# Optimization experiments

Measured on AMD Instinct MI355X. Metric: run time of the kernel, lower is better.

The kernel has to match this reference:

```python
import jax, jax.numpy as jnp
import numpy as np

HEADS = 8

def setup_inputs() -> dict:
    key = jax.random.key(0)
    ks = jax.random.split(key, 5)
    B, C, H, W = 2, 256, 64, 64
    dim = C
    x = jax.random.normal(ks[0], (B, C, H, W), dtype=jnp.float32)
    # Linear weights stored as [in, out] so y = x @ W + b
    w_qkv = jax.random.normal(ks[1], (dim, 3 * dim), dtype=jnp.float32) * (dim ** -0.5)
    b_qkv = jax.random.normal(ks[2], (3 * dim,), dtype=jnp.float32) * 0.02
    w_out = jax.random.normal(ks[3], (dim, dim), dtype=jnp.float32) * (dim ** -0.5)
    b_out = jax.random.normal(ks[4], (dim,), dtype=jnp.float32) * 0.02
    return {"x": x, "w_qkv": w_qkv, "b_qkv": b_qkv, "w_out": w_out, "b_out": b_out}

def reference(x, w_qkv, b_qkv, w_out, b_out):
    B, C, H, W = x.shape
    h = HEADS
    d = C // h
    scale = d ** -0.5
    # [B, C, H, W] -> [B, N, C]
    tokens = x.reshape(B, C, H * W).transpose(0, 2, 1)
    qkv = tokens @ w_qkv + b_qkv  # [B, N, 3C]
    q, k, v = jnp.split(qkv, 3, axis=-1)
    def to_heads(t):
        Bn, N, _ = t.shape
        return t.reshape(Bn, N, h, d).transpose(0, 2, 1, 3)  # [B, h, N, d]
    q, k, v = map(to_heads, (q, k, v))
    dots = jnp.einsum('bhnd,bhmd->bhnm', q, k) * scale  # [B, h, N, N]
    attn = jax.nn.softmax(dots, axis=-1)
    out = jnp.einsum('bhnm,bhmd->bhnd', attn, v)  # [B, h, N, d]
    out = out.transpose(0, 2, 1, 3).reshape(B, H * W, C)  # [B, N, C]
    out = out @ w_out + b_out
    return out.transpose(0, 2, 1).reshape(B, C, H, W)
```

## Files before the change

### kernel.cpp

```cpp
#include <hip/hip_runtime.h>

typedef __attribute__((ext_vector_type(8))) short s16x8;
typedef __attribute__((ext_vector_type(4))) short s16x4;
typedef __attribute__((ext_vector_type(4))) float f32x4;
typedef __attribute__((ext_vector_type(2))) unsigned u32x2;

#define MFMA32(a, b, c) __builtin_amdgcn_mfma_f32_16x16x32_bf16((a), (b), (c), 0, 0, 0)

#if __has_builtin(__builtin_amdgcn_mfma_f32_16x16x16bf16_1k)
#define MFMA16K(a, b, c) __builtin_amdgcn_mfma_f32_16x16x16bf16_1k((a), (b), (c), 0, 0, 0)
#else
#define MFMA16K(a, b, c) (c)
#endif

#if __has_builtin(__builtin_amdgcn_exp2f)
#define EXP2F(x) __builtin_amdgcn_exp2f(x)
#else
#define EXP2F(x) __exp2f(x)
#endif

#define SL2E 0.25507313f

__device__ __forceinline__ unsigned pkrne(float a, float b) {
  unsigned ua = __builtin_bit_cast(unsigned, a);
  unsigned ub = __builtin_bit_cast(unsigned, b);
  ua += 0x7FFFu + ((ua >> 16) & 1u);
  ub += 0x7FFFu + ((ub >> 16) & 1u);
  return __builtin_amdgcn_perm(ub, ua, 0x07060302u);
}

__device__ __forceinline__ unsigned pktrunc(float a, float b) {
  return __builtin_amdgcn_perm(__builtin_bit_cast(unsigned, b),
                               __builtin_bit_cast(unsigned, a), 0x07060302u);
}

__device__ __forceinline__ unsigned short bfr(float f) {
  unsigned u = __builtin_bit_cast(unsigned, f);
  u += 0x7FFFu + ((u >> 16) & 1u);
  return (unsigned short)(u >> 16);
}

__global__ __launch_bounds__(256) void prep_kernel(
    const float* __restrict__ x, const float* __restrict__ wqkv,
    const float* __restrict__ wout, ushort* __restrict__ xbf,
    ushort* __restrict__ wT, ushort* __restrict__ woT) {
  const int t = threadIdx.x;
  const int sub = t & 15, grp = t >> 4;
  const int id = blockIdx.x;
  const float* src;
  ushort* dst;
  int src_ld, k0, n0;
  float sc = 1.f;
  if (id < 512) {
    int mt = id & 63, kt = (id >> 6) & 3, b = id >> 8;
    src = x + (size_t)b * 256 * 4096;
    src_ld = 4096;
    dst = xbf + (size_t)b * 4096 * 256;
    k0 = kt * 64;
    n0 = mt * 64;
  } else if (id < 560) {
    int r = id - 512, nt = r % 12, kt = r / 12;
    src = wqkv;
    src_ld = 768;
    dst = wT;
    k0 = kt * 64;
    n0 = nt * 64;
    if (n0 < 256) sc = SL2E;
  } else {
    int r = id - 560, nt = r & 3, kt = r >> 2;
    src = wout;
    src_ld = 256;
    dst = woT;
    k0 = kt * 64;
    n0 = nt * 64;
  }
  const int k = k0 + grp * 4;
  const int n = n0 + sub * 4;
  unsigned d0[4], d1[4];
#pragma unroll
  for (int i = 0; i < 4; ++i) {
    float4 v = *(const float4*)(src + (size_t)(k + i) * src_ld + n);
    d0[i] = pkrne(v.x * sc, v.y * sc);
    d1[i] = pkrne(v.z * sc, v.w * sc);
  }
  u32x2 r0 = {__builtin_amdgcn_perm(d0[1], d0[0], 0x05040100u),
              __builtin_amdgcn_perm(d0[3], d0[2], 0x05040100u)};
  u32x2 r1 = {__builtin_amdgcn_perm(d0[1], d0[0], 0x07060302u),
              __builtin_amdgcn_perm(d0[3], d0[2], 0x07060302u)};
  u32x2 r2 = {__builtin_amdgcn_perm(d1[1], d1[0], 0x05040100u),
              __builtin_amdgcn_perm(d1[3], d1[2], 0x05040100u)};
  u32x2 r3 = {__builtin_amdgcn_perm(d1[1], d1[0], 0x07060302u),
              __builtin_amdgcn_perm(d1[3], d1[2], 0x07060302u)};
  *(u32x2*)(dst + (size_t)(n + 0) * 256 + k) = r0;
  *(u32x2*)(dst + (size_t)(n + 1) * 256 + k) = r1;
  *(u32x2*)(dst + (size_t)(n + 2) * 256 + k) = r2;
  *(u32x2*)(dst + (size_t)(n + 3) * 256 + k) = r3;
}

__global__ __launch_bounds__(256) void qkv_kernel(
    const ushort* __restrict__ xbf, const ushort* __restrict__ wT,
    const float* __restrict__ bq, ushort* __restrict__ QG,
    ushort* __restrict__ KG, ushort* __restrict__ VtG) {
  __shared__ __align__(16) ushort Wl[64][40];
  __shared__ __align__(16) ushort Xl[128][40];
  const int t0 = blockIdx.x * 128;
  const int n0 = blockIdx.y * 64;
  const int t = threadIdx.x;
  const int wid = t >> 6, lane = t & 63;
  const int wy = wid >> 1, wx = wid & 1;
  const int quad = lane >> 4, l16 = lane & 15;
  f32x4 acc[2][4] = {};
  const int wr = t >> 2, wsg = t & 3;
  for (int k0 = 0; k0 < 256; k0 += 32) {
    __syncthreads();
    *(uint4*)&Wl[wr][wsg * 8] =
        *(const uint4*)(wT + (size_t)(n0 + wr) * 256 + k0 + wsg * 8);
#pragma unroll
    for (int i = 0; i < 2; ++i) {
      int fid = t + 256 * i, row = fid >> 2, seg = fid & 3;
      *(uint4*)&Xl[row][seg * 8] =
          *(const uint4*)(xbf + (size_t)(t0 + row) * 256 + k0 + seg * 8);
    }
    __syncthreads();
    s16x8 wf[2], xf[4];
#pragma unroll
    for (int i = 0; i < 2; ++i)
      wf[i] = *(const s16x8*)&Wl[32 * wy + 16 * i + l16][quad * 8];
#pragma unroll
    for (int j = 0; j < 4; ++j)
      xf[j] = *(const s16x8*)&Xl[64 * wx + 16 * j + l16][quad * 8];
#pragma unroll
    for (int i = 0; i < 2; ++i)
#pragma unroll
      for (int j = 0; j < 4; ++j) acc[i][j] = MFMA32(wf[i], xf[j], acc[i][j]);
  }
  if (n0 < 512) {
    ushort* dst = (n0 < 256) ? QG : KG;
    const float bsc = (n0 < 256) ? SL2E : 1.f;
#pragma unroll
    for (int i = 0; i < 2; ++i) {
      int nb = n0 + 32 * wy + 16 * i + 4 * quad;
      float4 b4 = *(const float4*)(bq + nb);
      float bx0 = b4.x * bsc, bx1 = b4.y * bsc, bx2 = b4.z * bsc,
            bx3 = b4.w * bsc;
      int h = ((nb & 255) >> 5);
      int dd0 = nb & 31;
#pragma unroll
      for (int j = 0; j < 4; ++j) {
        int tok = t0 + 64 * wx + 16 * j + l16;
        int b = tok >> 12, tokn = tok & 4095;
        u32x2 pk = {pkrne(acc[i][j][0] + bx0, acc[i][j][1] + bx1),
                    pkrne(acc[i][j][2] + bx2, acc[i][j][3] + bx3)};
        *(u32x2*)(dst + ((size_t)(b * 8 + h) * 4096 + tokn) * 32 + dd0) = pk;
      }
    }
  } else {
#pragma unroll
    for (int i = 0; i < 2; ++i) {
      int nb = n0 + 32 * wy + 16 * i + 4 * quad;
      float4 b4 = *(const float4*)(bq + nb);
      float bb[4] = {b4.x, b4.y, b4.z, b4.w};
#pragma unroll
      for (int r = 0; r < 4; ++r) {
        int nn = nb + r - 512;
        int h = nn >> 5, ddv = nn & 31;
        ushort* vrow = VtG + (size_t)(h * 32 + ddv) * 4096;
#pragma unroll
        for (int j = 0; j < 4; ++j) {
          int tok = t0 + 64 * wx + 16 * j + l16;
          int b = tok >> 12, tokn = tok & 4095;
          vrow[(size_t)b * 8 * 32 * 4096 + tokn] = bfr(acc[i][j][r] + bb[r]);
        }
      }
    }
  }
}

__global__ __launch_bounds__(256) void attn_kernel(
    const ushort* __restrict__ QG, const ushort* __restrict__ KG,
    const ushort* __restrict__ VtG, ushort* __restrict__ Ob) {
  __shared__ __align__(16) ushort Kl[2][64][40];
  __shared__ __align__(16) ushort Vl[2][32][72];
  const int id = blockIdx.x;
  const int bh = (id & 7) * 2 + ((id >> 3) & 1);
  const int q0 = (id >> 4) * 128;
  const int t = threadIdx.x;
  const int wid = t >> 6, lane = t & 63;
  const int quad = lane >> 4, l16 = lane & 15;
  const size_t base = (size_t)bh * 4096 * 32;
  const ushort* qp = QG + base;
  const ushort* kp = KG + base;
  const ushort* vp = VtG + base;
  const int qw = q0 + 32 * wid;
  const s16x8 qf0 = *(const s16x8*)(qp + (size_t)(qw + l16) * 32 + quad * 8);
  const s16x8 qf1 = *(const s16x8*)(qp + (size_t)(qw + 16 + l16) * 32 + quad * 8);
  const int kr = t >> 2, ks = t & 3;
  const int vr = t >> 3, vsg = t & 7;
  *(uint4*)&Kl[0][kr][ks * 8] = *(const uint4*)(kp + (size_t)kr * 32 + ks * 8);
  *(uint4*)&Vl[0][vr][vsg * 8] = *(const uint4*)(vp + (size_t)vr * 4096 + vsg * 8);
  const ushort* kpre = kp + (size_t)(64 + kr) * 32 + ks * 8;
  const ushort* vpre = vp + (size_t)vr * 4096 + 64 + vsg * 8;
  __syncthreads();
  f32x4 o00 = {}, o01 = {}, o10 = {}, o11 = {}, ol0 = {}, ol1 = {};
  const f32x4 zero = {};
  const s16x4 ones = {(short)0x3F80, (short)0x3F80, (short)0x3F80,
                      (short)0x3F80};
#pragma unroll 2
  for (int kt = 0; kt < 64; ++kt) {
    const int cur = kt & 1;
    const bool more = (kt + 1) < 64;
    uint4 kv, vv;
    if (more) {
      kv = *(const uint4*)kpre;
      vv = *(const uint4*)vpre;
      kpre += 2048;
      vpre += 64;
    }
    f32x4 st0[4], st1[4];
#pragma unroll
    for (int nb = 0; nb < 4; ++nb) {
      s16x8 kf = *(const s16x8*)&Kl[cur][16 * nb + l16][quad * 8];
      st0[nb] = MFMA32(kf, qf0, zero);
      st1[nb] = MFMA32(kf, qf1, zero);
    }
    unsigned pl0[4], ph0[4], pl1[4], ph1[4];
#pragma unroll
    for (int nb = 0; nb < 4; ++nb) {
      float a0 = EXP2F(st0[nb][0]);
      float a1 = EXP2F(st0[nb][1]);
      float a2 = EXP2F(st0[nb][2]);
      float a3 = EXP2F(st0[nb][3]);
      pl0[nb] = pktrunc(a0, a1);
      ph0[nb] = pktrunc(a2, a3);
      float b0 = EXP2F(st1[nb][0]);
      float b1 = EXP2F(st1[nb][1]);
      float b2 = EXP2F(st1[nb][2]);
      float b3 = EXP2F(st1[nb][3]);
      pl1[nb] = pktrunc(b0, b1);
      ph1[nb] = pktrunc(b2, b3);
    }
#pragma unroll
    for (int nb = 0; nb < 4; ++nb) {
      u32x2 pu0 = {pl0[nb], ph0[nb]};
      u32x2 pu1 = {pl1[nb], ph1[nb]};
      s16x4 pv0 = __builtin_bit_cast(s16x4, pu0);
      s16x4 pv1 = __builtin_bit_cast(s16x4, pu1);
      s16x4 va = *(const s16x4*)&Vl[cur][l16][16 * nb + quad * 4];
      s16x4 vb = *(const s16x4*)&Vl[cur][16 + l16][16 * nb + quad * 4];
      o00 = MFMA16K(va, pv0, o00);
      o01 = MFMA16K(vb, pv0, o01);
      o10 = MFMA16K(va, pv1, o10);
      o11 = MFMA16K(vb, pv1, o11);
      ol0 = MFMA16K(ones, pv0, ol0);
      ol1 = MFMA16K(ones, pv1, ol1);
    }
    if (more) {
      *(uint4*)&Kl[cur ^ 1][kr][ks * 8] = kv;
      *(uint4*)&Vl[cur ^ 1][vr][vsg * 8] = vv;
    }
    __syncthreads();
  }
  const float inv0 = 1.0f / ol0[0];
  const float inv1 = 1.0f / ol1[0];
  const int b = bh >> 3, h = bh & 7;
  const int tok0 = qw + l16;
  const size_t row0 = ((size_t)b * 4096 + tok0) * 256 + h * 32;
  const size_t row1 = row0 + (size_t)16 * 256;
  u32x2 w00 = {pkrne(o00[0] * inv0, o00[1] * inv0),
               pkrne(o00[2] * inv0, o00[3] * inv0)};
  u32x2 w01 = {pkrne(o01[0] * inv0, o01[1] * inv0),
               pkrne(o01[2] * inv0, o01[3] * inv0)};
  u32x2 w10 = {pkrne(o10[0] * inv1, o10[1] * inv1),
               pkrne(o10[2] * inv1, o10[3] * inv1)};
  u32x2 w11 = {pkrne(o11[0] * inv1, o11[1] * inv1),
               pkrne(o11[2] * inv1, o11[3] * inv1)};
  *(u32x2*)(Ob + row0 + 4 * quad) = w00;
  *(u32x2*)(Ob + row0 + 16 + 4 * quad) = w01;
  *(u32x2*)(Ob + row1 + 4 * quad) = w10;
  *(u32x2*)(Ob + row1 + 16 + 4 * quad) = w11;
}

__global__ __launch_bounds__(256) void proj_kernel(
    const ushort* __restrict__ Ob, const ushort* __restrict__ woT,
    const float* __restrict__ bo, float* __restrict__ out) {
  __shared__ __align__(16) ushort Wl[64][40];
  __shared__ __align__(16) ushort Xl[128][40];
  const int t0 = blockIdx.x * 128;
  const int c0 = blockIdx.y * 64;
  const int t = threadIdx.x;
  const int wid = t >> 6, lane = t & 63;
  const int wy = wid >> 1, wx = wid & 1;
  const int quad = lane >> 4, l16 = lane & 15;
  f32x4 acc[2][4] = {};
  const int wr = t >> 2, wsg = t & 3;
  for (int k0 = 0; k0 < 256; k0 += 32) {
    __syncthreads();
    *(uint4*)&Wl[wr][wsg * 8] =
        *(const uint4*)(woT + (size_t)(c0 + wr) * 256 + k0 + wsg * 8);
#pragma unroll
    for (int i = 0; i < 2; ++i) {
      int fid = t + 256 * i, row = fid >> 2, seg = fid & 3;
      *(uint4*)&Xl[row][seg * 8] =
          *(const uint4*)(Ob + (size_t)(t0 + row) * 256 + k0 + seg * 8);
    }
    __syncthreads();
    s16x8 wf[2], xf[4];
#pragma unroll
    for (int i = 0; i < 2; ++i)
      wf[i] = *(const s16x8*)&Wl[32 * wy + 16 * i + l16][quad * 8];
#pragma unroll
    for (int j = 0; j < 4; ++j)
      xf[j] = *(const s16x8*)&Xl[64 * wx + 16 * j + l16][quad * 8];
#pragma unroll
    for (int i = 0; i < 2; ++i)
#pragma unroll
      for (int j = 0; j < 4; ++j) acc[i][j] = MFMA32(wf[i], xf[j], acc[i][j]);
  }
#pragma unroll
  for (int i = 0; i < 2; ++i) {
    int cb = c0 + 32 * wy + 16 * i + 4 * quad;
    float4 b4 = *(const float4*)(bo + cb);
    float bb[4] = {b4.x, b4.y, b4.z, b4.w};
#pragma unroll
    for (int j = 0; j < 4; ++j) {
      int tok = t0 + 64 * wx + 16 * j + l16;
      int b = tok >> 12, tokn = tok & 4095;
#pragma unroll
      for (int r = 0; r < 4; ++r)
        out[((size_t)(b * 256 + cb + r)) * 4096 + tokn] = acc[i][j][r] + bb[r];
    }
  }
}

extern "C" void kernel_launch(void* const* d_in, const int* in_sizes, int n_in,
                              void* d_out, int out_size, void* d_ws, size_t ws_size,
                              hipStream_t stream) {
  (void)in_sizes; (void)n_in; (void)out_size; (void)ws_size;
  const float* x = (const float*)d_in[0];
  const float* wq = (const float*)d_in[1];
  const float* bq = (const float*)d_in[2];
  const float* wo = (const float*)d_in[3];
  const float* bo = (const float*)d_in[4];
  float* out = (float*)d_out;
  ushort* ws = (ushort*)d_ws;
  ushort* xbf = ws;
  ushort* Ob  = ws;
  ushort* QG  = ws + 2097152;
  ushort* KG  = ws + 4194304;
  ushort* VtG = ws + 6291456;
  ushort* wT  = ws + 8388608;
  ushort* woT = ws + 8585216;
  prep_kernel<<<576, 256, 0, stream>>>(x, wq, wo, xbf, wT, woT);
  qkv_kernel<<<dim3(64, 12), 256, 0, stream>>>(xbf, wT, bq, QG, KG, VtG);
  attn_kernel<<<512, 256, 0, stream>>>(QG, KG, VtG, Ob);
  proj_kernel<<<dim3(64, 4), 256, 0, stream>>>(Ob, woT, bo, out);
}
```

Measured before the change: 147.6 us.

## Split attention over two key halves and merge partials in projection kernel

Attention now splits the key range into two halves, launching twice as many blocks (1024), each writing unnormalized fp32 partial outputs and row sums to workspace. The projection kernel merges the two partials, normalizes with a reciprocal, converts to bf16 and then does the output GEMM. This aims to raise occupancy and parallelism on the attention stage, which had only 512 blocks. In exchange it adds extra fp32 global traffic for the partials and more work in the projection load path. The split path only runs if the workspace is large enough, otherwise the old kernels are used.

Result: faster. 144.0 us (-2.4%).

```diff
diff --git a/kernel.cpp b/kernel.cpp
--- a/kernel.cpp
+++ b/kernel.cpp
@@ -17,6 +17,12 @@
 #define EXP2F(x) __builtin_amdgcn_exp2f(x)
 #else
 #define EXP2F(x) __exp2f(x)
+#endif
+
+#if __has_builtin(__builtin_amdgcn_rcpf)
+#define RCPF(x) __builtin_amdgcn_rcpf(x)
+#else
+#define RCPF(x) (1.0f / (x))
 #endif
 
 #define SL2E 0.25507313f
@@ -176,7 +182,173 @@
   }
 }
 
-__global__ __launch_bounds__(256) void attn_kernel(
+__global__ __launch_bounds__(256) void attn_split(
+    const ushort* __restrict__ QG, const ushort* __restrict__ KG,
+    const ushort* __restrict__ VtG, float* __restrict__ OF,
+    float* __restrict__ LF) {
+  __shared__ __align__(16) ushort Kl[2][64][40];
+  __shared__ __align__(16) ushort Vl[2][32][72];
+  const int id = blockIdx.x;
+  const int bh = (id & 7) * 2 + ((id >> 3) & 1);
+  const int q0 = ((id >> 4) & 31) * 128;
+  const int sp = id >> 9;
+  const int kt0 = sp * 32, kt1 = kt0 + 32;
+  const int t = threadIdx.x;
+  const int wid = t >> 6, lane = t & 63;
+  const int quad = lane >> 4, l16 = lane & 15;
+  const size_t base = (size_t)bh * 4096 * 32;
+  const ushort* qp = QG + base;
+  const ushort* kp = KG + base;
+  const ushort* vp = VtG + base;
+  const int qw = q0 + 32 * wid;
+  const s16x8 qf0 = *(const s16x8*)(qp + (size_t)(qw + l16) * 32 + quad * 8);
+  const s16x8 qf1 = *(const s16x8*)(qp + (size_t)(qw + 16 + l16) * 32 + quad * 8);
+  const int kr = t >> 2, ks = t & 3;
+  const int vr = t >> 3, vsg = t & 7;
+  *(uint4*)&Kl[0][kr][ks * 8] =
+      *(const uint4*)(kp + (size_t)(kt0 * 64 + kr) * 32 + ks * 8);
+  *(uint4*)&Vl[0][vr][vsg * 8] =
+      *(const uint4*)(vp + (size_t)vr * 4096 + kt0 * 64 + vsg * 8);
+  const ushort* kpre = kp + (size_t)((kt0 + 1) * 64 + kr) * 32 + ks * 8;
+  const ushort* vpre = vp + (size_t)vr * 4096 + (kt0 + 1) * 64 + vsg * 8;
+  __syncthreads();
+  f32x4 o00 = {}, o01 = {}, o10 = {}, o11 = {}, ol0 = {}, ol1 = {};
+  const f32x4 zero = {};
+  const s16x4 ones = {(short)0x3F80, (short)0x3F80, (short)0x3F80,
+                      (short)0x3F80};
+#pragma unroll 2
+  for (int kt = kt0; kt < kt1; ++kt) {
+    const int cur = kt & 1;
+    const bool more = (kt + 1) < kt1;
+    uint4 kv, vv;
+    if (more) {
+      kv = *(const uint4*)kpre;
+      vv = *(const uint4*)vpre;
+      kpre += 2048;
+      vpre += 64;
+    }
+    f32x4 st0[4], st1[4];
+#pragma unroll
+    for (int nb = 0; nb < 4; ++nb) {
+      s16x8 kf = *(const s16x8*)&Kl[cur][16 * nb + l16][quad * 8];
+      st0[nb] = MFMA32(kf, qf0, zero);
+      st1[nb] = MFMA32(kf, qf1, zero);
+    }
+    unsigned pl0[4], ph0[4], pl1[4], ph1[4];
+#pragma unroll
+    for (int nb = 0; nb < 4; ++nb) {
+      float a0 = EXP2F(st0[nb][0]);
+      float a1 = EXP2F(st0[nb][1]);
+      float a2 = EXP2F(st0[nb][2]);
+      float a3 = EXP2F(st0[nb][3]);
+      pl0[nb] = pktrunc(a0, a1);
+      ph0[nb] = pktrunc(a2, a3);
+      float b0 = EXP2F(st1[nb][0]);
+      float b1 = EXP2F(st1[nb][1]);
+      float b2 = EXP2F(st1[nb][2]);
+      float b3 = EXP2F(st1[nb][3]);
+      pl1[nb] = pktrunc(b0, b1);
+      ph1[nb] = pktrunc(b2, b3);
+    }
+#pragma unroll
+    for (int nb = 0; nb < 4; ++nb) {
+      u32x2 pu0 = {pl0[nb], ph0[nb]};
+      u32x2 pu1 = {pl1[nb], ph1[nb]};
+      s16x4 pv0 = __builtin_bit_cast(s16x4, pu0);
+      s16x4 pv1 = __builtin_bit_cast(s16x4, pu1);
+      s16x4 va = *(const s16x4*)&Vl[cur][l16][16 * nb + quad * 4];
+      s16x4 vb = *(const s16x4*)&Vl[cur][16 + l16][16 * nb + quad * 4];
+      o00 = MFMA16K(va, pv0, o00);
+      o01 = MFMA16K(vb, pv0, o01);
+      o10 = MFMA16K(va, pv1, o10);
+      o11 = MFMA16K(vb, pv1, o11);
+      ol0 = MFMA16K(ones, pv0, ol0);
+      ol1 = MFMA16K(ones, pv1, ol1);
+    }
+    if (more) {
+      *(uint4*)&Kl[cur ^ 1][kr][ks * 8] = kv;
+      *(uint4*)&Vl[cur ^ 1][vr][vsg * 8] = vv;
+    }
+    __syncthreads();
+  }
+  float* OFs = OF + (size_t)sp * 2097152;
+  float* LFs = LF + (size_t)sp * 65536;
+  const int tok0 = qw + l16;
+  const size_t ob0 = ((size_t)bh * 4096 + tok0) * 32;
+  const size_t ob1 = ob0 + (size_t)16 * 32;
+  *(f32x4*)(OFs + ob0 + 4 * quad) = o00;
+  *(f32x4*)(OFs + ob0 + 16 + 4 * quad) = o01;
+  *(f32x4*)(OFs + ob1 + 4 * quad) = o10;
+  *(f32x4*)(OFs + ob1 + 16 + 4 * quad) = o11;
+  if (quad == 0) {
+    LFs[(size_t)bh * 4096 + tok0] = ol0[0];
+    LFs[(size_t)bh * 4096 + tok0 + 16] = ol1[0];
+  }
+}
+
+__global__ __launch_bounds__(256) void proj_split(
+    const float* __restrict__ OF, const float* __restrict__ LF,
+    const ushort* __restrict__ woT, const float* __restrict__ bo,
+    float* __restrict__ out) {
+  __shared__ __align__(16) ushort Wl[64][40];
+  __shared__ __align__(16) ushort Xl[128][40];
+  const int t0 = blockIdx.x * 128;
+  const int c0 = blockIdx.y * 64;
+  const int t = threadIdx.x;
+  const int wid = t >> 6, lane = t & 63;
+  const int wy = wid >> 1, wx = wid & 1;
+  const int quad = lane >> 4, l16 = lane & 15;
+  f32x4 acc[2][4] = {};
+  const int wr = t >> 2, wsg = t & 3;
+  const int c8 = (t & 7) * 4;
+  for (int k0 = 0; k0 < 256; k0 += 32) {
+    __syncthreads();
+    *(uint4*)&Wl[wr][wsg * 8] =
+        *(const uint4*)(woT + (size_t)(c0 + wr) * 256 + k0 + wsg * 8);
+    const int hh = k0 >> 5;
+#pragma unroll
+    for (int p = 0; p < 4; ++p) {
+      int row = 32 * p + (t >> 3);
+      int tok = t0 + row, bb = tok >> 12, tokn = tok & 4095;
+      size_t ro = (size_t)(bb * 8 + hh) * 4096 + tokn;
+      f32x4 v0 = *(const f32x4*)(OF + ro * 32 + c8);
+      f32x4 v1 = *(const f32x4*)(OF + 2097152 + ro * 32 + c8);
+      float l = LF[ro] + LF[65536 + ro];
+      float inv = RCPF(l);
+      f32x4 s = (v0 + v1) * inv;
+      u32x2 pk = {pkrne(s[0], s[1]), pkrne(s[2], s[3])};
+      *(u32x2*)&Xl[row][c8] = pk;
+    }
+    __syncthreads();
+    s16x8 wf[2], xf[4];
+#pragma unroll
+    for (int i = 0; i < 2; ++i)
+      wf[i] = *(const s16x8*)&Wl[32 * wy + 16 * i + l16][quad * 8];
+#pragma unroll
+    for (int j = 0; j < 4; ++j)
+      xf[j] = *(const s16x8*)&Xl[64 * wx + 16 * j + l16][quad * 8];
+#pragma unroll
+    for (int i = 0; i < 2; ++i)
+#pragma unroll
+      for (int j = 0; j < 4; ++j) acc[i][j] = MFMA32(wf[i], xf[j], acc[i][j]);
+  }
+#pragma unroll
+  for (int i = 0; i < 2; ++i) {
+    int cb = c0 + 32 * wy + 16 * i + 4 * quad;
+    float4 b4 = *(const float4*)(bo + cb);
+    float bb[4] = {b4.x, b4.y, b4.z, b4.w};
+#pragma unroll
+    for (int j = 0; j < 4; ++j) {
+      int tok = t0 + 64 * wx + 16 * j + l16;
+      int b = tok >> 12, tokn = tok & 4095;
+#pragma unroll
+      for (int r = 0; r < 4; ++r)
+        out[((size_t)(b * 256 + cb + r)) * 4096 + tokn] = acc[i][j][r] + bb[r];
+    }
+  }
+}
+
+__global__ __launch_bounds__(256) void attn_fb(
     const ushort* __restrict__ QG, const ushort* __restrict__ KG,
     const ushort* __restrict__ VtG, ushort* __restrict__ Ob) {
   __shared__ __align__(16) ushort Kl[2][64][40];
@@ -280,7 +452,7 @@
   *(u32x2*)(Ob + row1 + 16 + 4 * quad) = w11;
 }
 
-__global__ __launch_bounds__(256) void proj_kernel(
+__global__ __launch_bounds__(256) void proj_fb(
     const ushort* __restrict__ Ob, const ushort* __restrict__ woT,
     const float* __restrict__ bo, float* __restrict__ out) {
   __shared__ __align__(16) ushort Wl[64][40];
@@ -335,7 +507,7 @@
 extern "C" void kernel_launch(void* const* d_in, const int* in_sizes, int n_in,
                               void* d_out, int out_size, void* d_ws, size_t ws_size,
                               hipStream_t stream) {
-  (void)in_sizes; (void)n_in; (void)out_size; (void)ws_size;
+  (void)in_sizes; (void)n_in; (void)out_size;
   const float* x = (const float*)d_in[0];
   const float* wq = (const float*)d_in[1];
   const float* bq = (const float*)d_in[2];
@@ -350,8 +522,16 @@
   ushort* VtG = ws + 6291456;
   ushort* wT  = ws + 8388608;
   ushort* woT = ws + 8585216;
+  float* OF = (float*)(ws + 8650752);
+  float* LF = OF + 4194304;
+  const bool split = ws_size >= 34603008;
   prep_kernel<<<576, 256, 0, stream>>>(x, wq, wo, xbf, wT, woT);
   qkv_kernel<<<dim3(64, 12), 256, 0, stream>>>(xbf, wT, bq, QG, KG, VtG);
-  attn_kernel<<<512, 256, 0, stream>>>(QG, KG, VtG, Ob);
-  proj_kernel<<<dim3(64, 4), 256, 0, stream>>>(Ob, woT, bo, out);
-}
+  if (split) {
+    attn_split<<<1024, 256, 0, stream>>>(QG, KG, VtG, OF, LF);
+    proj_split<<<dim3(64, 4), 256, 0, stream>>>(OF, LF, woT, bo, out);
+  } else {
+    attn_fb<<<512, 256, 0, stream>>>(QG, KG, VtG, Ob);
+    proj_fb<<<dim3(64, 4), 256, 0, stream>>>(Ob, woT, bo, out);
+  }
+}
```

## Split attention KV range three ways and merge partials in projection

Applied to the files above, without the earlier changes.

The attention kernel now splits the key/value sequence into three chunks (split-K), launching 1536 blocks instead of 512. Each block writes unnormalized bf16 partial outputs and row sums, with no max subtraction needed since exponentials are unshifted. The projection kernel loads the three partials, sums them, normalizes by the combined row sum and then runs its GEMM. This is meant to fill the MI355X CUs better (512 blocks is only about two per CU), at the cost of extra partial-output traffic, bf16 rounding of partials, and a fused merge in the projection load path.

Measured after the change: 141.5 us. 1.04x faster.

```diff
diff --git a/kernel.cpp b/kernel.cpp
--- a/kernel.cpp
+++ b/kernel.cpp
@@ -17,6 +17,12 @@
 #define EXP2F(x) __builtin_amdgcn_exp2f(x)
 #else
 #define EXP2F(x) __exp2f(x)
+#endif
+
+#if __has_builtin(__builtin_amdgcn_rcpf)
+#define RCPF(x) __builtin_amdgcn_rcpf(x)
+#else
+#define RCPF(x) (1.0f / (x))
 #endif
 
 #define SL2E 0.25507313f
@@ -38,6 +44,13 @@
   unsigned u = __builtin_bit_cast(unsigned, f);
   u += 0x7FFFu + ((u >> 16) & 1u);
   return (unsigned short)(u >> 16);
+}
+
+__device__ __forceinline__ float bflo(unsigned u) {
+  return __builtin_bit_cast(float, u << 16);
+}
+__device__ __forceinline__ float bfhi(unsigned u) {
+  return __builtin_bit_cast(float, u & 0xFFFF0000u);
 }
 
 __global__ __launch_bounds__(256) void prep_kernel(
@@ -176,14 +189,18 @@
   }
 }
 
-__global__ __launch_bounds__(256) void attn_kernel(
+__global__ __launch_bounds__(256, 6) void attn_split(
     const ushort* __restrict__ QG, const ushort* __restrict__ KG,
-    const ushort* __restrict__ VtG, ushort* __restrict__ Ob) {
+    const ushort* __restrict__ VtG, ushort* __restrict__ OF0,
+    ushort* __restrict__ OFb, float* __restrict__ LF) {
   __shared__ __align__(16) ushort Kl[2][64][40];
   __shared__ __align__(16) ushort Vl[2][32][72];
   const int id = blockIdx.x;
   const int bh = (id & 7) * 2 + ((id >> 3) & 1);
-  const int q0 = (id >> 4) * 128;
+  const int q0 = ((id >> 4) & 31) * 128;
+  const int sp = id >> 9;
+  const int kt0 = (sp * 64 + 2) / 3;
+  const int niter = ((sp + 1) * 64 + 2) / 3 - kt0;
   const int t = threadIdx.x;
   const int wid = t >> 6, lane = t & 63;
   const int quad = lane >> 4, l16 = lane & 15;
@@ -196,19 +213,20 @@
   const s16x8 qf1 = *(const s16x8*)(qp + (size_t)(qw + 16 + l16) * 32 + quad * 8);
   const int kr = t >> 2, ks = t & 3;
   const int vr = t >> 3, vsg = t & 7;
-  *(uint4*)&Kl[0][kr][ks * 8] = *(const uint4*)(kp + (size_t)kr * 32 + ks * 8);
-  *(uint4*)&Vl[0][vr][vsg * 8] = *(const uint4*)(vp + (size_t)vr * 4096 + vsg * 8);
-  const ushort* kpre = kp + (size_t)(64 + kr) * 32 + ks * 8;
-  const ushort* vpre = vp + (size_t)vr * 4096 + 64 + vsg * 8;
+  *(uint4*)&Kl[0][kr][ks * 8] =
+      *(const uint4*)(kp + (size_t)(kt0 * 64 + kr) * 32 + ks * 8);
+  *(uint4*)&Vl[0][vr][vsg * 8] =
+      *(const uint4*)(vp + (size_t)vr * 4096 + kt0 * 64 + vsg * 8);
+  const ushort* kpre = kp + (size_t)((kt0 + 1) * 64 + kr) * 32 + ks * 8;
+  const ushort* vpre = vp + (size_t)vr * 4096 + (kt0 + 1) * 64 + vsg * 8;
   __syncthreads();
   f32x4 o00 = {}, o01 = {}, o10 = {}, o11 = {}, ol0 = {}, ol1 = {};
   const f32x4 zero = {};
   const s16x4 ones = {(short)0x3F80, (short)0x3F80, (short)0x3F80,
                       (short)0x3F80};
-#pragma unroll 2
-  for (int kt = 0; kt < 64; ++kt) {
-    const int cur = kt & 1;
-    const bool more = (kt + 1) < 64;
+  for (int i = 0; i < niter; ++i) {
+    const int cur = i & 1;
+    const bool more = (i + 1) < niter;
     uint4 kv, vv;
     if (more) {
       kv = *(const uint4*)kpre;
@@ -216,28 +234,16 @@
       kpre += 2048;
       vpre += 64;
     }
-    f32x4 st0[4], st1[4];
+    unsigned pl0[4], ph0[4], pl1[4], ph1[4];
 #pragma unroll
     for (int nb = 0; nb < 4; ++nb) {
       s16x8 kf = *(const s16x8*)&Kl[cur][16 * nb + l16][quad * 8];
-      st0[nb] = MFMA32(kf, qf0, zero);
-      st1[nb] = MFMA32(kf, qf1, zero);
-    }
-    unsigned pl0[4], ph0[4], pl1[4], ph1[4];
-#pragma unroll
-    for (int nb = 0; nb < 4; ++nb) {
-      float a0 = EXP2F(st0[nb][0]);
-      float a1 = EXP2F(st0[nb][1]);
-      float a2 = EXP2F(st0[nb][2]);
-      float a3 = EXP2F(st0[nb][3]);
-      pl0[nb] = pktrunc(a0, a1);
-      ph0[nb] = pktrunc(a2, a3);
-      float b0 = EXP2F(st1[nb][0]);
-      float b1 = EXP2F(st1[nb][1]);
-      float b2 = EXP2F(st1[nb][2]);
-      float b3 = EXP2F(st1[nb][3]);
-      pl1[nb] = pktrunc(b0, b1);
-      ph1[nb] = pktrunc(b2, b3);
+      f32x4 s0 = MFMA32(kf, qf0, zero);
+      f32x4 s1 = MFMA32(kf, qf1, zero);
+      pl0[nb] = pktrunc(EXP2F(s0[0]), EXP2F(s0[1]));
+      ph0[nb] = pktrunc(EXP2F(s0[2]), EXP2F(s0[3]));
+      pl1[nb] = pktrunc(EXP2F(s1[0]), EXP2F(s1[1]));
+      ph1[nb] = pktrunc(EXP2F(s1[2]), EXP2F(s1[3]));
     }
 #pragma unroll
     for (int nb = 0; nb < 4; ++nb) {
@@ -260,28 +266,28 @@
     }
     __syncthreads();
   }
-  const float inv0 = 1.0f / ol0[0];
-  const float inv1 = 1.0f / ol1[0];
-  const int b = bh >> 3, h = bh & 7;
+  ushort* OFs = (sp == 0) ? OF0 : OFb + (size_t)(sp - 1) * 2097152;
+  float* LFs = LF + (size_t)sp * 65536;
   const int tok0 = qw + l16;
-  const size_t row0 = ((size_t)b * 4096 + tok0) * 256 + h * 32;
-  const size_t row1 = row0 + (size_t)16 * 256;
-  u32x2 w00 = {pkrne(o00[0] * inv0, o00[1] * inv0),
-               pkrne(o00[2] * inv0, o00[3] * inv0)};
-  u32x2 w01 = {pkrne(o01[0] * inv0, o01[1] * inv0),
-               pkrne(o01[2] * inv0, o01[3] * inv0)};
-  u32x2 w10 = {pkrne(o10[0] * inv1, o10[1] * inv1),
-               pkrne(o10[2] * inv1, o10[3] * inv1)};
-  u32x2 w11 = {pkrne(o11[0] * inv1, o11[1] * inv1),
-               pkrne(o11[2] * inv1, o11[3] * inv1)};
-  *(u32x2*)(Ob + row0 + 4 * quad) = w00;
-  *(u32x2*)(Ob + row0 + 16 + 4 * quad) = w01;
-  *(u32x2*)(Ob + row1 + 4 * quad) = w10;
-  *(u32x2*)(Ob + row1 + 16 + 4 * quad) = w11;
-}
-
-__global__ __launch_bounds__(256) void proj_kernel(
-    const ushort* __restrict__ Ob, const ushort* __restrict__ woT,
+  const size_t ob0 = ((size_t)bh * 4096 + tok0) * 32;
+  const size_t ob1 = ob0 + (size_t)16 * 32;
+  u32x2 w00 = {pkrne(o00[0], o00[1]), pkrne(o00[2], o00[3])};
+  u32x2 w01 = {pkrne(o01[0], o01[1]), pkrne(o01[2], o01[3])};
+  u32x2 w10 = {pkrne(o10[0], o10[1]), pkrne(o10[2], o10[3])};
+  u32x2 w11 = {pkrne(o11[0], o11[1]), pkrne(o11[2], o11[3])};
+  *(u32x2*)(OFs + ob0 + 4 * quad) = w00;
+  *(u32x2*)(OFs + ob0 + 16 + 4 * quad) = w01;
+  *(u32x2*)(OFs + ob1 + 4 * quad) = w10;
+  *(u32x2*)(OFs + ob1 + 16 + 4 * quad) = w11;
+  if (quad == 0) {
+    LFs[(size_t)bh * 4096 + tok0] = ol0[0];
+    LFs[(size_t)bh * 4096 + tok0 + 16] = ol1[0];
+  }
+}
+
+__global__ __launch_bounds__(256) void proj_split(
+    const ushort* __restrict__ OF0, const ushort* __restrict__ OFb,
+    const float* __restrict__ LF, const ushort* __restrict__ woT,
     const float* __restrict__ bo, float* __restrict__ out) {
   __shared__ __align__(16) ushort Wl[64][40];
   __shared__ __align__(16) ushort Xl[128][40];
@@ -293,15 +299,31 @@
   const int quad = lane >> 4, l16 = lane & 15;
   f32x4 acc[2][4] = {};
   const int wr = t >> 2, wsg = t & 3;
+  const int c8 = (t & 7) * 4;
   for (int k0 = 0; k0 < 256; k0 += 32) {
     __syncthreads();
     *(uint4*)&Wl[wr][wsg * 8] =
         *(const uint4*)(woT + (size_t)(c0 + wr) * 256 + k0 + wsg * 8);
-#pragma unroll
-    for (int i = 0; i < 2; ++i) {
-      int fid = t + 256 * i, row = fid >> 2, seg = fid & 3;
-      *(uint4*)&Xl[row][seg * 8] =
-          *(const uint4*)(Ob + (size_t)(t0 + row) * 256 + k0 + seg * 8);
+    const int hh = k0 >> 5;
+#pragma unroll
+    for (int p = 0; p < 4; ++p) {
+      int row = 32 * p + (t >> 3);
+      int tok = t0 + row, bb = tok >> 12, tokn = tok & 4095;
+      size_t ro = (size_t)(bb * 8 + hh) * 4096 + tokn;
+      size_t oi = ro * 32 + c8;
+      uint2 a0 = *(const uint2*)(OF0 + oi);
+      uint2 a1 = *(const uint2*)(OFb + oi);
+      uint2 a2 = *(const uint2*)(OFb + 2097152 + oi);
+      float l = LF[ro] + LF[65536 + ro] + LF[131072 + ro];
+      float inv = RCPF(l);
+      f32x4 s;
+      s[0] = bflo(a0.x) + bflo(a1.x) + bflo(a2.x);
+      s[1] = bfhi(a0.x) + bfhi(a1.x) + bfhi(a2.x);
+      s[2] = bflo(a0.y) + bflo(a1.y) + bflo(a2.y);
+      s[3] = bfhi(a0.y) + bfhi(a1.y) + bfhi(a2.y);
+      s *= inv;
+      u32x2 pk = {pkrne(s[0], s[1]), pkrne(s[2], s[3])};
+      *(u32x2*)&Xl[row][c8] = pk;
     }
     __syncthreads();
     s16x8 wf[2], xf[4];
@@ -344,14 +366,16 @@
   float* out = (float*)d_out;
   ushort* ws = (ushort*)d_ws;
   ushort* xbf = ws;
-  ushort* Ob  = ws;
+  ushort* OF0 = ws;
   ushort* QG  = ws + 2097152;
   ushort* KG  = ws + 4194304;
   ushort* VtG = ws + 6291456;
   ushort* wT  = ws + 8388608;
   ushort* woT = ws + 8585216;
+  ushort* OFb = ws + 8650752;
+  float* LF = (float*)(ws + 12845056);
   prep_kernel<<<576, 256, 0, stream>>>(x, wq, wo, xbf, wT, woT);
   qkv_kernel<<<dim3(64, 12), 256, 0, stream>>>(xbf, wT, bq, QG, KG, VtG);
-  attn_kernel<<<512, 256, 0, stream>>>(QG, KG, VtG, Ob);
-  proj_kernel<<<dim3(64, 4), 256, 0, stream>>>(Ob, woT, bo, out);
-}
+  attn_split<<<1536, 256, 0, stream>>>(QG, KG, VtG, OF0, OFb, LF);
+  proj_split<<<dim3(64, 4), 256, 0, stream>>>(OF0, OFb, LF, woT, bo, out);
+}
```
